# Kernel optimization log

Hardware: AMD Instinct MI355X
Metric: run time of the kernel (lower is better)

Reference implementation:

```python
import jax, jax.numpy as jnp
import numpy as np

DN = ('NCHW', 'OIHW', 'NCHW')
B, HP, LR = 4, 256, 64  # batch, pan side length, lrms side length


def conv(x, w):
    return jax.lax.conv_general_dilated(x, w, (1, 1), 'SAME', dimension_numbers=DN)


def gauss_k(ks, sigma):
    i = np.arange(ks) - (ks - 1) / 2.0
    k = np.exp(-(i * i) / (2.0 * sigma * sigma))
    k /= k.sum()
    return jnp.asarray(k, jnp.float32)


def gaussian_hp(x, ks, sigma):
    # Faithful to source: cv2.GaussianBlur is applied ONLY to channel 0 of each
    # sample; remaining channels get lp == x, hence hp == 0. Separable blur with
    # reflect-101 padding (cv2 default border).
    k = gauss_k(ks, sigma)
    p = ks // 2
    x0 = x[:, :1]
    y = jnp.pad(x0, ((0, 0), (0, 0), (p, p), (0, 0)), mode='reflect')
    y = jax.lax.conv_general_dilated(y, k.reshape(1, 1, ks, 1), (1, 1), 'VALID', dimension_numbers=DN)
    y = jnp.pad(y, ((0, 0), (0, 0), (0, 0), (p, p)), mode='reflect')
    y = jax.lax.conv_general_dilated(y, k.reshape(1, 1, 1, ks), (1, 1), 'VALID', dimension_numbers=DN)
    hp0 = x0 - y
    if x.shape[1] > 1:
        hp0 = jnp.concatenate([hp0, jnp.zeros_like(x[:, 1:])], axis=1)
    return hp0


def pixel_shuffle(x, r):
    b, c, h, w = x.shape
    x = x.reshape(b, c // (r * r), r, r, h, w)
    return x.transpose(0, 1, 4, 2, 5, 3).reshape(b, c // (r * r), h * r, w * r)


def hornet(x, w1, w2):
    return conv(jax.nn.gelu(conv(x, w1)), w2)


def ffc(x, wl2l, wl2g, wg2l, wspec):
    # ratio 0.5/0.5 split -> 8 local / 8 global channels
    xl, xg = x[:, :8], x[:, 8:]
    l2l, l2g, g2l = conv(xl, wl2l), conv(xl, wl2g), conv(xg, wg2l)
    f = jnp.fft.rfft2(xg, axes=(2, 3), norm='ortho')
    z = jnp.concatenate([f.real, f.imag], axis=1)
    z = jax.nn.relu(conv(z, wspec))
    g2g = jnp.fft.irfft2(z[:, :8] + 1j * z[:, 8:], s=xg.shape[2:], axes=(2, 3), norm='ortho')
    return l2l, l2g, g2l, g2g


def refine(x, win, wb1, wb2, wca1, wca2, wout):
    # RCAB-style refinement: conv-in, residual body with channel attention, conv-out
    y = conv(x, win)
    bdy = conv(jax.nn.relu(conv(y, wb1)), wb2)
    ca = jax.nn.sigmoid(conv(jax.nn.relu(conv(bdy.mean((2, 3), keepdims=True), wca1)), wca2))
    return conv(y + bdy * ca, wout)


def coord1d(n):
    r = 1.0 / n
    return -1.0 + r + 2.0 * r * jnp.arange(n, dtype=jnp.float32)


def mlp(x, w_in, b_in, w_h, b_h, w_out, b_out):
    h = jax.nn.relu(x @ w_in + b_in)
    for i in range(w_h.shape[0]):
        h = jax.nn.relu(h @ w_h[i] + b_h[i])
    return h @ w_out + b_out


def liif(feat, coord, cell, w_in, b_in, w_h, b_h, w_out, b_out):
    # LIIF with feat_unfold=True, local_ensemble=True, cell_decode=True
    b, c, h, w = feat.shape
    fp = jnp.pad(feat, ((0, 0), (0, 0), (1, 1), (1, 1)))
    patches = jnp.concatenate([fp[:, :, i:i + h, j:j + w] for i in range(3) for j in range(3)], axis=1)
    pf = patches.reshape(b, 9 * c, h * w)  # [B, 144, H*W]
    cy, cx = coord1d(h), coord1d(w)
    rx, ry = 1.0 / h, 1.0 / w
    preds, areas = [], []
    for vx in (-1.0, 1.0):
        for vy in (-1.0, 1.0):
            c0 = jnp.clip(coord[..., 0] + vx * rx + 1e-6, -1 + 1e-6, 1 - 1e-6)
            c1 = jnp.clip(coord[..., 1] + vy * ry + 1e-6, -1 + 1e-6, 1 - 1e-6)
            i0 = jnp.clip(jnp.floor((c0 + 1.0) * h / 2.0).astype(jnp.int32), 0, h - 1)
            i1 = jnp.clip(jnp.floor((c1 + 1.0) * w / 2.0).astype(jnp.int32), 0, w - 1)
            idx = i0 * w + i1  # [B, Q]
            q = jnp.take_along_axis(pf, idx[:, None, :], axis=2).transpose(0, 2, 1)  # [B,Q,144]
            rel0 = (coord[..., 0] - cy[i0]) * h
            rel1 = (coord[..., 1] - cx[i1]) * w
            inp = jnp.concatenate([q, rel0[..., None], rel1[..., None],
                                   cell[..., :1] * h, cell[..., 1:] * w], axis=-1)
            preds.append(mlp(inp, w_in, b_in, w_h, b_h, w_out, b_out))
            areas.append(jnp.abs(rel0 * rel1) + 1e-9)
    areas[0], areas[3] = areas[3], areas[0]
    areas[1], areas[2] = areas[2], areas[1]
    tot = areas[0] + areas[1] + areas[2] + areas[3]
    return sum(p * (a / tot)[..., None] for p, a in zip(preds, areas))


def _forward(lrms, pan, w_conv_ps, hor_w1, hor_w2, ffc_l2l, ffc_l2g, ffc_g2l, ffc_spec,
             ref_in, ref_b1, ref_b2, ref_ca1, ref_ca2, ref_out,
             w_fuse, w_liif, w_hp, mlp_w_in, mlp_b_in, mlp_w_h, mlp_b_h, mlp_w_out, mlp_b_out):
    side = pan.shape[-1]
    c1 = coord1d(side)
    grid = jnp.stack(jnp.meshgrid(c1, c1, indexing='ij'), -1).reshape(-1, 2)
    coord = jnp.broadcast_to(grid[None], (pan.shape[0], side * side, 2))
    cell = jnp.full_like(coord, 2.0 / side)

    lrms_up = pixel_shuffle(conv(lrms, w_conv_ps), 4)

    blur_cfg = [(5, 1.5), (27, 2.0), (41, 2.8)]
    R = lambda i: (ref_in[i], ref_b1[i], ref_b2[i], ref_ca1[i], ref_ca2[i], ref_out[i])
    Fc = lambda i: (ffc_l2l[i], ffc_l2g[i], ffc_g2l[i], ffc_spec[i])

    fused = []
    for br in range(3):
        ks, sg = blur_cfg[br]
        feat = jnp.concatenate([gaussian_hp(pan, ks, sg), gaussian_hp(lrms_up, ks, sg)], axis=1)
        feat = hornet(feat, hor_w1[br], hor_w2[br])
        f0 = refine(feat, *R(3 * br))
        l2l, l2g, g2l, g2g = ffc(f0, *Fc(2 * br))
        f1 = refine(jnp.concatenate([l2g + g2g, l2l + g2l], axis=1), *R(3 * br + 1))
        l2l, l2g, g2l, g2g = ffc(f1, *Fc(2 * br + 1))
        f2 = refine(jnp.concatenate([l2g + g2g, l2l + g2l], axis=1), *R(3 * br + 2))
        fused.append(conv(jnp.concatenate([f0, f1, f2], axis=1), w_fuse[br]))

    feat_all = conv(jnp.concatenate(fused, axis=1), w_liif)
    fo = liif(feat_all, coord, cell, mlp_w_in, mlp_b_in, mlp_w_h, mlp_b_h, mlp_w_out, mlp_b_out)
    fo = fo.transpose(0, 2, 1).reshape(pan.shape[0], -1, side, side)
    return conv(fo, w_hp) + lrms_up


def setup_inputs() -> dict:
    key = jax.random.key(0)
    ks = jax.random.split(key, 24)
    n = lambda i, shape, s=0.05: jax.random.normal(ks[i], shape, jnp.float32) * s
    return dict(
        lrms=n(0, (B, 4, LR, LR), 1.0),
        pan=n(1, (B, 1, HP, HP), 1.0),
        w_conv_ps=n(2, (64, 4, 3, 3)),
        hor_w1=n(3, (3, 16, 5, 3, 3)),
        hor_w2=n(4, (3, 16, 16, 3, 3)),
        ffc_l2l=n(5, (6, 8, 8, 3, 3)),
        ffc_l2g=n(6, (6, 8, 8, 3, 3)),
        ffc_g2l=n(7, (6, 8, 8, 3, 3)),
        ffc_spec=n(8, (6, 16, 16, 1, 1), 0.1),
        ref_in=n(9, (9, 16, 16, 3, 3)),
        ref_b1=n(10, (9, 16, 16, 3, 3)),
        ref_b2=n(11, (9, 16, 16, 3, 3)),
        ref_ca1=n(12, (9, 4, 16, 1, 1), 0.1),
        ref_ca2=n(13, (9, 16, 4, 1, 1), 0.1),
        ref_out=n(14, (9, 16, 16, 3, 3)),
        w_fuse=n(15, (3, 16, 48, 1, 1), 0.1),
        w_liif=n(16, (16, 48, 1, 1), 0.1),
        w_hp=n(17, (4, 16, 3, 3)),
        mlp_w_in=n(18, (148, 256), 148 ** -0.5),
        mlp_b_in=jnp.zeros((256,), jnp.float32),
        mlp_w_h=n(19, (3, 256, 256), 256 ** -0.5),
        mlp_b_h=jnp.zeros((3, 256), jnp.float32),
        mlp_w_out=n(20, (256, 16), 256 ** -0.5),
        mlp_b_out=jnp.zeros((16,), jnp.float32),
    )


def reference(lrms, pan, w_conv_ps, hor_w1, hor_w2, ffc_l2l, ffc_l2g, ffc_g2l, ffc_spec,
              ref_in, ref_b1, ref_b2, ref_ca1, ref_ca2, ref_out,
              w_fuse, w_liif, w_hp, mlp_w_in, mlp_b_in, mlp_w_h, mlp_b_h, mlp_w_out, mlp_b_out):
    return _forward(lrms, pan, w_conv_ps, hor_w1, hor_w2, ffc_l2l, ffc_l2g, ffc_g2l, ffc_spec,
                    ref_in, ref_b1, ref_b2, ref_ca1, ref_ca2, ref_out,
                    w_fuse, w_liif, w_hp, mlp_w_in, mlp_b_in, mlp_w_h, mlp_b_h, mlp_w_out, mlp_b_out)
```

## Files before the change

### kernel.cpp

```cpp
#include <hip/hip_runtime.h>
#include <hip/hip_bf16.h>
#include <math.h>

typedef __hip_bfloat16 bf16;
typedef __attribute__((ext_vector_type(8))) short short8;
typedef __attribute__((ext_vector_type(4))) short short4v;
typedef __attribute__((ext_vector_type(4))) float float4v;

#define ACT_NONE 0
#define ACT_RELU 1
#define ACT_GELU 2

__device__ __forceinline__ float b2f(bf16 v){ return __bfloat162float(v); }
__device__ __forceinline__ bf16  f2b(float f){ return __float2bfloat16(f); }
__device__ __forceinline__ short f2bs(float f){ bf16 h = __float2bfloat16(f); return *reinterpret_cast<short*>(&h); }
__device__ __forceinline__ float bs2f(short s){ return __uint_as_float(((unsigned)(unsigned short)s) << 16); }
__device__ __forceinline__ void rotc(float& tr, float& ti, float cr, float ci){
    float t = tr*cr - ti*ci; ti = tr*ci + ti*cr; tr = t;
}

struct GK3 { float k[3][41]; int ks[3]; };

__global__ __launch_bounds__(256) void conv_ps_k(const float* __restrict__ lrms,
                                                 const float* __restrict__ w,
                                                 float* __restrict__ up){
    int tid = threadIdx.x, bx = blockIdx.x;
    int y = bx & 255, c = (bx >> 8) & 3, b = bx >> 10;
    int x = tid;
    int h = y >> 2, r1 = y & 3, ww = x >> 2, r2 = x & 3;
    int oc = c*16 + r1*4 + r2;
    float acc = 0.f;
    for (int ic = 0; ic < 4; ++ic) {
        const float* base = lrms + ((b*4 + ic) << 12);
        const float* wb = w + (oc*4 + ic)*9;
        #pragma unroll
        for (int ky = 0; ky < 3; ++ky) {
            int hh = h + ky - 1; if (hh < 0 || hh > 63) continue;
            #pragma unroll
            for (int kx = 0; kx < 3; ++kx) {
                int cc = ww + kx - 1; if (cc < 0 || cc > 63) continue;
                acc += base[(hh<<6) + cc] * wb[ky*3 + kx];
            }
        }
    }
    up[(((size_t)(b*4 + c)) << 16) + (y<<8) + x] = acc;
}

__global__ __launch_bounds__(256) void gauss_hp_k(const float* __restrict__ pan,
                                                  const float* __restrict__ lrms_up,
                                                  bf16* __restrict__ feat2, GK3 g){
    int tid = threadIdx.x, bx = blockIdx.x;
    int y = bx & 255, b = (bx >> 8) & 3, src = (bx >> 10) & 1, br = bx >> 11;
    int ks = g.ks[br], p = ks >> 1;
    const float* gk = g.k[br];
    const float* s = src ? (lrms_up + (size_t)b*4*65536) : (pan + (size_t)b*65536);
    __shared__ float vext[296];
    for (int i = tid; i < 296; i += 256) {
        int xe = i - 20; int xr = xe < 0 ? -xe : (xe > 255 ? 510 - xe : xe);
        float acc = 0.f;
        for (int t = 0; t < ks; ++t) {
            int yy = y - p + t; yy = yy < 0 ? -yy : (yy > 255 ? 510 - yy : yy);
            acc += gk[t] * s[(yy<<8) + xr];
        }
        vext[i] = acc;
    }
    __syncthreads();
    int x = tid;
    float acc = 0.f;
    for (int t = 0; t < ks; ++t) acc += gk[t] * vext[x - p + t + 20];
    float o = s[(y<<8) + x];
    feat2[(((size_t)((br*4 + b)*2 + src)) << 16) + (y<<8) + x] = f2b(o - acc);
}

__global__ __launch_bounds__(256) void convA_k(const bf16* __restrict__ in, int inCper, int Cin,
                                               const float* __restrict__ wbase, int wbrstride, int wocstride,
                                               bf16* __restrict__ out, int act){
    int tid = threadIdx.x, bx = blockIdx.x;
    int y = bx & 255, b = (bx >> 8) & 3, br = bx >> 10;
    const float* w = wbase + (size_t)br * wbrstride;
    int x = tid;
    float acc[16];
    #pragma unroll
    for (int oc = 0; oc < 16; ++oc) acc[oc] = 0.f;
    for (int ic = 0; ic < Cin; ++ic) {
        const bf16* base = in + ((size_t)((br*4 + b)*inCper + ic) << 16);
        const float* wic = w + ic*9;
        #pragma unroll
        for (int ky = 0; ky < 3; ++ky) {
            int yy = y + ky - 1; if (yy < 0 || yy > 255) continue;
            const bf16* rowp = base + (yy<<8);
            float v0 = (x > 0)   ? b2f(rowp[x-1]) : 0.f;
            float v1 = b2f(rowp[x]);
            float v2 = (x < 255) ? b2f(rowp[x+1]) : 0.f;
            const float* wr = wic + ky*3;
            #pragma unroll
            for (int oc = 0; oc < 16; ++oc) {
                const float* wo = wr + oc*wocstride;
                acc[oc] = fmaf(wo[0], v0, fmaf(wo[1], v1, fmaf(wo[2], v2, acc[oc])));
            }
        }
    }
    #pragma unroll
    for (int oc = 0; oc < 16; ++oc) {
        float a = acc[oc];
        if (act == ACT_RELU) a = fmaxf(a, 0.f);
        else if (act == ACT_GELU) {
            float u = 0.7978845608028654f * (a + 0.044715f*a*a*a);
            a = 0.5f * a * (1.f + tanhf(u));
        }
        out[((size_t)((br*4 + b)*16 + oc) << 16) + (y<<8) + x] = f2b(a);
    }
}

__global__ __launch_bounds__(256) void pack_all_k(const float* __restrict__ mw_in,
        const float* __restrict__ mw_h, const float* __restrict__ mw_out,
        const float* __restrict__ hor_w2,
        const float* __restrict__ ref_in, const float* __restrict__ ref_b1,
        const float* __restrict__ ref_b2, const float* __restrict__ ref_out,
        const float* __restrict__ l2l, const float* __restrict__ l2g,
        const float* __restrict__ g2l,
        short* __restrict__ wp, short* __restrict__ wc){
    int idx = blockIdx.x*256 + threadIdx.x;
    const int S0 = 40960, SH = 65536;
    const int TOTM = S0 + 3*SH + 4096;
    const int TOTC = 45*2560;
    if (idx < TOTM) {
        float val;
        if (idx < S0) {
            int j = idx & 7, l = (idx>>3) & 63, nt = (idx>>9) & 15, kt = idx >> 13;
            int k = kt*32 + (l>>4)*8 + j;
            int n = nt*16 + (l&15);
            val = (k < 148) ? mw_in[k*256 + n] : 0.f;
        } else if (idx < S0 + 3*SH) {
            int i2 = idx - S0;
            int L = i2 >> 16, r = i2 & 65535;
            int j = r & 7, l = (r>>3) & 63, nt = (r>>9) & 15, kt = r >> 13;
            int k = kt*32 + (l>>4)*8 + j;
            int n = nt*16 + (l&15);
            val = mw_h[L*65536 + k*256 + n];
        } else {
            int i3 = idx - S0 - 3*SH;
            int j = i3 & 7, l = (i3>>3) & 63, kt = i3 >> 9;
            int k = kt*32 + (l>>4)*8 + j;
            int oc = l & 15;
            val = mw_out[k*16 + oc];
// ... 13 lines not shown
        int tap = k >> 4, ic = k & 15;
        if (g == 10 || g == 11) {
            int wi = 2*br + (g-10);
            if (n < 8) v = (ic < 8) ? l2g[((wi*8 + n)*8 + ic)*9 + tap] : 0.f;
            else {
                int o = n - 8;
                v = (ic < 8) ? l2l[((wi*8 + o)*8 + ic)*9 + tap]
                             : g2l[((wi*8 + o)*8 + (ic-8))*9 + tap];
            }
        } else {
            int widx = (n*16 + ic)*9 + tap;
            const float* src;
            if (g == 0)       src = hor_w2 + br*2304;
            else if (g <= 3)  src = ref_in + (3*br + (g-1))*2304;
            else if (g <= 6)  src = ref_b1 + (3*br + (g-4))*2304;
            else if (g <= 9)  src = ref_b2 + (3*br + (g-7))*2304;
            else              src = ref_out + (3*br + (g-12))*2304;
            v = src[widx];
        }
    }
    wc[idx2] = f2bs(v);
}

__global__ __launch_bounds__(256) void convM_k(const bf16* __restrict__ in,
        const short* __restrict__ wgroup,
        bf16* __restrict__ out, int act, float* __restrict__ means){
    __shared__ short sIn[6*258*20];
    __shared__ float sm[4][16];
    int tid = threadIdx.x, bx = blockIdx.x;
    int y0 = (bx & 63) << 2, b = (bx >> 6) & 3, br = bx >> 8;
    size_t pbase = (size_t)((br*4 + b)*16) << 16;
    if (tid < 192) {
        int r = tid >> 5, side = (tid >> 4) & 1, ic = tid & 15;
        sIn[(r*258 + (side ? 257 : 0))*20 + ic] = 0;
    }
    {
        int g = tid >> 5, tl = tid & 31, x0 = tl << 3, ic0 = g*2;
        for (int r = 0; r < 6; ++r) {
            int yy = y0 - 1 + r;
            short8 lo = {0,0,0,0,0,0,0,0}, hi = {0,0,0,0,0,0,0,0};
            if (yy >= 0 && yy <= 255) {
                lo = *(const short8*)&in[pbase + ((size_t)ic0<<16) + (yy<<8) + x0];
                hi = *(const short8*)&in[pbase + ((size_t)(ic0+1)<<16) + (yy<<8) + x0];
            }
            #pragma unroll
            for (int t = 0; t < 8; ++t) {
// ... 169 lines not shown
    }
    #pragma unroll
    for (int mt = 0; mt < 16; ++mt) {
        short8 a2 = {0,0,0,0,0,0,0,0};
        if (q < 2) a2 = *(const short8*)&sF[(mt*16 + m_l)*16 + q*8];
        float4v d2 = (float4v){0.f,0.f,0.f,0.f};
        d2 = __builtin_amdgcn_mfma_f32_16x16x32_bf16(a2, b2, d2, 0, 0, 0);
        size_t fidx = ((size_t)(b*48 + br*16 + m_l) << 16) + (yrow<<8) + mt*16 + q*4;
        short4v pk;
        if (step == 0) {
            #pragma unroll
            for (int r = 0; r < 4; ++r) pk[r] = f2bs(d2[r]);
        } else {
            short4v old = *(const short4v*)&fusedCat[fidx];
            #pragma unroll
            for (int r = 0; r < 4; ++r) pk[r] = f2bs(bs2f(old[r]) + d2[r]);
        }
        *(short4v*)&fusedCat[fidx] = pk;
    }
}

__global__ __launch_bounds__(256) void rfft_wT_k(const bf16* __restrict__ F,
                                                 bf16* __restrict__ ore, bf16* __restrict__ oim){
    __shared__ float rows[16][256];
    __shared__ float Ar[256], Ai[256];
    __shared__ float Tr[129][17], Ti[129][17];
    int tid = threadIdx.x, bx = blockIdx.x;
    int t = bx & 15, c = (bx >> 4) & 7, b = (bx >> 7) & 3, br = bx >> 9;
    int y0 = t << 4;
    size_t plane = (size_t)((br*4 + b)*16 + 8 + c) << 16;
    #pragma unroll
    for (int r = 0; r < 16; ++r)
        rows[r][tid] = b2f(F[plane + ((size_t)(y0 + r) << 8) + tid]);
    __syncthreads();
    int n1 = tid >> 4, k1 = tid & 15;
    float a1 = -6.283185307179586f * (float)k1 / 16.f;
    float c1, s1; __sincosf(a1, &s1, &c1);
    float a2 = -6.283185307179586f * (float)tid / 256.f;
    float c2v, s2v; __sincosf(a2, &s2v, &c2v);
    for (int r = 0; r < 16; ++r) {
        float twr = 1.f, twi = 0.f, ar = 0.f, ai = 0.f;
        #pragma unroll
        for (int n2 = 0; n2 < 16; ++n2) {
            float xr = rows[r][n1 + (n2<<4)];
            ar = fmaf(xr, twr, ar); ai = fmaf(xr, twi, ai);
            rotc(twr, twi, c1, s1);
        }
        Ar[tid] = ar; Ai[tid] = ai;
        __syncthreads();
        float t2r = 1.f, t2i = 0.f, re = 0.f, im = 0.f;
        #pragma unroll
        for (int m = 0; m < 16; ++m) {
            float rr = Ar[(m<<4) + k1], ii = Ai[(m<<4) + k1];
            re += rr*t2r - ii*t2i; im += ii*t2r + rr*t2i;
            rotc(t2r, t2i, c2v, s2v);
        }
        if (tid < 129) { Tr[tid][r] = re * 0.0625f; Ti[tid][r] = im * 0.0625f; }
        __syncthreads();
    }
    size_t obase = ((size_t)(((br*4 + b)*8 + c)*129)) * 256 + y0;
    for (int idx = tid; idx < 129*16; idx += 256) {
        int k = idx >> 4, ty = idx & 15;
        ore[obase + (size_t)k*256 + ty] = f2b(Tr[k][ty]);
        oim[obase + (size_t)k*256 + ty] = f2b(Ti[k][ty]);
    }
}

__global__ __launch_bounds__(256) void fftspec_hT_k(const bf16* __restrict__ re0, const bf16* __restrict__ im0,
                                                    const float* __restrict__ wspec, int step,
                                                    bf16* __restrict__ re1, bf16* __restrict__ im1){
    __shared__ float Fr[8][256], Fi[8][256], Sr[8][256], Si[8][256], Ar[256], Ai[256];
    int tid = threadIdx.x, bx = blockIdx.x;
    int k = bx % 129; int r2 = bx / 129; int b = r2 & 3, br = r2 >> 2;
    size_t cb = (size_t)((br*4 + b)*8) * 33024 + (size_t)k * 256;
    int n1 = tid >> 4, k1 = tid & 15;
    float a1 = -6.283185307179586f * (float)k1 / 16.f;
    float c1, s1; __sincosf(a1, &s1, &c1);
    float a2 = -6.283185307179586f * (float)tid / 256.f;
    float c2v, s2v; __sincosf(a2, &s2v, &c2v);
    #pragma unroll
    for (int c = 0; c < 8; ++c) {
        size_t base = cb + (size_t)c*33024 + tid;
        Fr[c][tid] = b2f(re0[base]);
        Fi[c][tid] = b2f(im0[base]);
    }
    __syncthreads();
    for (int c = 0; c < 8; ++c) {
        float twr = 1.f, twi = 0.f, ar = 0.f, ai = 0.f;
        #pragma unroll
        for (int n2 = 0; n2 < 16; ++n2) {
            float r = Fr[c][n1 + (n2<<4)], i = Fi[c][n1 + (n2<<4)];
            ar += r*twr - i*twi; ai += i*twr + r*twi;
            rotc(twr, twi, c1, s1);
        }
        Ar[tid] = ar; Ai[tid] = ai;
        __syncthreads();
        float t2r = 1.f, t2i = 0.f, rr = 0.f, ii = 0.f;
        #pragma unroll
        for (int m = 0; m < 16; ++m) {
            float r = Ar[(m<<4) + k1], i = Ai[(m<<4) + k1];
            rr += r*t2r - i*t2i; ii += i*t2r + r*t2i;
            rotc(t2r, t2i, c2v, s2v);
        }
        Sr[c][tid] = rr * 0.0625f; Si[c][tid] = ii * 0.0625f;
        __syncthreads();
    }
    {
        const float* wl = wspec + (2*br + step)*256;
        float outv[16];
        #pragma unroll
        for (int oc = 0; oc < 16; ++oc) {
            float acc = 0.f;
            #pragma unroll
            for (int ic = 0; ic < 8; ++ic)
                acc += Sr[ic][tid] * wl[oc*16 + ic] + Si[ic][tid] * wl[oc*16 + 8 + ic];
            outv[oc] = fmaxf(acc, 0.f);
        }
        __syncthreads();
        #pragma unroll
        for (int oc = 0; oc < 8; ++oc) { Fr[oc][tid] = outv[oc]; Fi[oc][tid] = outv[oc+8]; }
        __syncthreads();
    }
    for (int c = 0; c < 8; ++c) {
        float twr = 1.f, twi = 0.f, ar = 0.f, ai = 0.f;
        #pragma unroll
        for (int n2 = 0; n2 < 16; ++n2) {
            float r = Fr[c][n1 + (n2<<4)], i = Fi[c][n1 + (n2<<4)];
            ar += r*twr + i*twi;
            ai += i*twr - r*twi;
            rotc(twr, twi, c1, s1);
        }
        Ar[tid] = ar; Ai[tid] = ai;
        __syncthreads();
        float t2r = 1.f, t2i = 0.f, rr = 0.f, ii = 0.f;
        #pragma unroll
        for (int m = 0; m < 16; ++m) {
            float r = Ar[(m<<4) + k1], i = Ai[(m<<4) + k1];
            rr += r*t2r + i*t2i;
            ii += i*t2r - r*t2i;
            rotc(t2r, t2i, c2v, s2v);
        }
        size_t base = cb + (size_t)c*33024 + tid;
        re1[base] = f2b(rr * 0.0625f);
        im1[base] = f2b(ii * 0.0625f);
        __syncthreads();
    }
}

__global__ __launch_bounds__(256) void irfft_wT_k(const bf16* __restrict__ re1, const bf16* __restrict__ im1,
                                                  bf16* __restrict__ A){
    __shared__ float Cr[129][17], Ci[129][17];
    __shared__ float er[256], ei[256];
    __shared__ float Ar[256], Ai[256];
    int tid = threadIdx.x, bx = blockIdx.x;
    int t = bx & 15, c = (bx >> 4) & 7, b = (bx >> 7) & 3, br = bx >> 9;
    int y0 = t << 4;
    size_t ibase = ((size_t)(((br*4 + b)*8 + c)*129)) * 256 + y0;
    for (int idx = tid; idx < 129*16; idx += 256) {
        int k = idx >> 4, ty = idx & 15;
        Cr[k][ty] = b2f(re1[ibase + (size_t)k*256 + ty]);
        Ci[k][ty] = (k == 0 || k == 128) ? 0.f : b2f(im1[ibase + (size_t)k*256 + ty]);
    }
    __syncthreads();
    int n1 = tid >> 4, k1 = tid & 15;
    float a1 = 6.283185307179586f * (float)k1 / 16.f;
    float c1, s1; __sincosf(a1, &s1, &c1);
    float a2 = 6.283185307179586f * (float)tid / 256.f;
    float c2v, s2v; __sincosf(a2, &s2v, &c2v);
    size_t plane = (size_t)((br*4 + b)*16 + c) << 16;
    for (int ty = 0; ty < 16; ++ty) {
        if (tid < 129) { er[tid] = Cr[tid][ty]; ei[tid] = Ci[tid][ty]; }
        else           { er[tid] = Cr[256 - tid][ty]; ei[tid] = -Ci[256 - tid][ty]; }
        __syncthreads();
        float twr = 1.f, twi = 0.f, ar = 0.f, ai = 0.f;
        #pragma unroll
        for (int n2 = 0; n2 < 16; ++n2) {
            float r = er[n1 + (n2<<4)], i = ei[n1 + (n2<<4)];
            ar += r*twr - i*twi; ai += i*twr + r*twi;
            rotc(twr, twi, c1, s1);
        }
        Ar[tid] = ar; Ai[tid] = ai;
        __syncthreads();
        float t2r = 1.f, t2i = 0.f, racc = 0.f;
        #pragma unroll
        for (int m = 0; m < 16; ++m) {
            float r = Ar[(m<<4) + k1], i = Ai[(m<<4) + k1];
            racc += r*t2r - i*t2i;
            rotc(t2r, t2i, c2v, s2v);
        }
        size_t o = plane + ((size_t)(y0 + ty) << 8) + tid;
        A[o] = f2b(b2f(A[o]) + racc * 0.0625f);
        __syncthreads();
    }
}

__global__ __launch_bounds__(256) void fuse1x1_k(const bf16* __restrict__ fc, const float* __restrict__ wl,
                                                 bf16* __restrict__ feat_all){
    int tid = threadIdx.x, bx = blockIdx.x;
    int pt = bx & 255, b = bx >> 8;
    int p = (pt << 8) + tid;
    float acc[16];
    #pragma unroll
    for (int oc = 0; oc < 16; ++oc) acc[oc] = 0.f;
    for (int ic = 0; ic < 48; ++ic) {
        float v = b2f(fc[((size_t)(b*48 + ic) << 16) + p]);
        #pragma unroll
        for (int oc = 0; oc < 16; ++oc) acc[oc] = fmaf(wl[oc*48 + ic], v, acc[oc]);
    }
    #pragma unroll
    for (int oc = 0; oc < 16; ++oc)
        feat_all[((size_t)(b*16 + oc) << 16) + p] = f2b(acc[oc]);
}

__global__ __launch_bounds__(256) void mlp_mfma_k(const short* __restrict__ feat,
        const short* __restrict__ wp,
        const float* __restrict__ b_in, const float* __restrict__ b_h,
        const float* __restrict__ b_out,
        float* __restrict__ fo){
    extern __shared__ short act_s[];
    int tid = threadIdx.x, bx = blockIdx.x;
    long P0 = (long)bx * 64;
    for (int idx = tid; idx < 64*160; idx += 256) {
        int pp = idx / 160, j = idx - pp*160;
        long P = P0 + pp;
        int bb = (int)(P >> 16), pim = (int)(P & 65535);
        int s0 = pim >> 8, s1 = pim & 255;
        short v = 0;
        if (j < 144) {
            int iy = j/48, ix = (j>>4)%3, c2 = j&15;
            int yy = s0 + iy - 1, xx = s1 + ix - 1;
            if (yy >= 0 && yy < 256 && xx >= 0 && xx < 256)
                v = feat[(((long)(bb*16 + c2)) << 16) + (yy<<8) + xx];
        } else if (j == 146 || j == 147) v = 0x4000;
        act_s[pp*264 + j] = v;
    }
    __syncthreads();

    int l = tid & 63, w = tid >> 6;
    int m_l = l & 15, q = l >> 4;
    int ntb = w*4;
    const short* wph  = wp + 40960;
    const short* wpo  = wp + 40960 + 3*65536;

    float4v acc[4][4];
    #pragma unroll
    for (int mt = 0; mt < 4; ++mt)
        #pragma unroll
        for (int nt = 0; nt < 4; ++nt) acc[mt][nt] = (float4v){0.f,0.f,0.f,0.f};
    for (int kt = 0; kt < 5; ++kt) {
        const short* bp = wp + ((size_t)(kt*16 + ntb)*64 + l)*8;
        short8 bfr[4];
        #pragma unroll
        for (int nt = 0; nt < 4; ++nt) bfr[nt] = *(const short8*)(bp + (size_t)nt*64*8);
        #pragma unroll
        for (int mt = 0; mt < 4; ++mt) {
            short8 a = *(const short8*)&act_s[(mt*16 + m_l)*264 + kt*32 + q*8];
            #pragma unroll
            for (int nt = 0; nt < 4; ++nt)
                acc[mt][nt] = __builtin_amdgcn_mfma_f32_16x16x32_bf16(a, bfr[nt], acc[mt][nt], 0, 0, 0);
        }
    }
    __syncthreads();
    #pragma unroll
    for (int nt = 0; nt < 4; ++nt) {
        int n = (ntb + nt)*16 + m_l;
        float bias = b_in[n];
        #pragma unroll
        for (int mt = 0; mt < 4; ++mt)
            #pragma unroll
            for (int r = 0; r < 4; ++r) {
                float vv = fmaxf(acc[mt][nt][r] + bias, 0.f);
                act_s[(mt*16 + q*4 + r)*264 + n] = f2bs(vv);
            }
    }
    __syncthreads();
    for (int L = 0; L < 3; ++L) {
        #pragma unroll
        for (int mt = 0; mt < 4; ++mt)
            #pragma unroll
            for (int nt = 0; nt < 4; ++nt) acc[mt][nt] = (float4v){0.f,0.f,0.f,0.f};
        const short* wl = wph + (size_t)L * 65536;
        for (int kt = 0; kt < 8; ++kt) {
            const short* bp = wl + ((size_t)(kt*16 + ntb)*64 + l)*8;
            short8 bfr[4];
            #pragma unroll
            for (int nt = 0; nt < 4; ++nt) bfr[nt] = *(const short8*)(bp + (size_t)nt*64*8);
            #pragma unroll
            for (int mt = 0; mt < 4; ++mt) {
                short8 a = *(const short8*)&act_s[(mt*16 + m_l)*264 + kt*32 + q*8];
                #pragma unroll
                for (int nt = 0; nt < 4; ++nt)
                    acc[mt][nt] = __builtin_amdgcn_mfma_f32_16x16x32_bf16(a, bfr[nt], acc[mt][nt], 0, 0, 0);
            }
        }
        __syncthreads();
        #pragma unroll
        for (int nt = 0; nt < 4; ++nt) {
            int n = (ntb + nt)*16 + m_l;
            float bias = b_h[L*256 + n];
            #pragma unroll
            for (int mt = 0; mt < 4; ++mt)
                #pragma unroll
                for (int r = 0; r < 4; ++r) {
                    float vv = fmaxf(acc[mt][nt][r] + bias, 0.f);
                    act_s[(mt*16 + q*4 + r)*264 + n] = f2bs(vv);
                }
        }
        __syncthreads();
    }
    if (w == 0) {
        float4v o[4];
        #pragma unroll
        for (int mt = 0; mt < 4; ++mt) o[mt] = (float4v){0.f,0.f,0.f,0.f};
        for (int kt = 0; kt < 8; ++kt) {
            short8 bf = *(const short8*)(wpo + ((size_t)kt*64 + l)*8);
// ... 22 lines not shown
        const short* __restrict__ wp,
        const float* __restrict__ b_in, const float* __restrict__ b_h,
        const float* __restrict__ b_out,
        float* __restrict__ fo){
    extern __shared__ short act_s[];
    int tid = threadIdx.x, bx = blockIdx.x;
    int E0 = bx * 128;
    for (int idx = tid; idx < 128*160; idx += 256) {
        int pp = idx / 160, j = idx - pp*160;
        int e = E0 + pp; if (e >= 6132) e = 0;
        int bb = e / 1533; int rem = e - bb*1533;
        int cn = rem / 511; int eidx = rem - cn*511;
        int s0 = (eidx < 256) ? 255 : eidx - 256;
        int s1 = (eidx < 256) ? eidx : 255;
        int vx = (cn == 0) ? -1 : 1;
        int vy = (cn == 1) ? -1 : 1;
        int i0 = (vx > 0) ? min(s0+1, 255) : s0;
        int i1 = (vy > 0) ? min(s1+1, 255) : s1;
        short v = 0;
        if (j < 144) {
            int iy = j/48, ix = (j>>4)%3, c2 = j&15;
            int yy = i0 + iy - 1, xx = i1 + ix - 1;
            if (yy >= 0 && yy < 256 && xx >= 0 && xx < 256)
                v = feat[(((long)(bb*16 + c2)) << 16) + (yy<<8) + xx];
        } else if (j == 144) v = f2bs(2.f*(float)(s0 - i0));
        else if (j == 145) v = f2bs(2.f*(float)(s1 - i1));
        else if (j >= 146) v = 0x4000;
        act_s[pp*264 + j] = v;
    }
    __syncthreads();

    int l = tid & 63, w = tid >> 6;
    int m_l = l & 15, q = l >> 4;
    int row0 = w * 32;
    const short* wph  = wp + 40960;
    const short* wpo  = wp + 40960 + 3*65536;

    float4v acc[2][16];
    #pragma unroll
    for (int mt = 0; mt < 2; ++mt)
        #pragma unroll
        for (int nt = 0; nt < 16; ++nt) acc[mt][nt] = (float4v){0.f,0.f,0.f,0.f};
    for (int kt = 0; kt < 5; ++kt) {
        short8 a0 = *(const short8*)&act_s[(row0 + m_l)*264 + kt*32 + q*8];
        short8 a1 = *(const short8*)&act_s[(row0 + 16 + m_l)*264 + kt*32 + q*8];
        const short* bp = wp + ((size_t)(kt*16)*64 + l)*8;
        #pragma unroll
// ... 125 lines not shown

    const size_t PLANE = 65536;
    char* base = (char*)d_ws;
    size_t off = 0;
    auto alloc = [&](size_t bytes){ void* p = base + off; off += (bytes + 255) & ~(size_t)255; return p; };
    float* lrms_up  = (float*)alloc(16*PLANE*4);
    bf16*  feat2    = (bf16*) alloc(24*PLANE*2);
    bf16*  bA       = (bf16*) alloc(192*PLANE*2);
    bf16*  bB       = (bf16*) alloc(192*PLANE*2);
    bf16*  bC       = (bf16*) alloc(192*PLANE*2);
    bf16*  bF       = (bf16*) alloc(192*PLANE*2);
    bf16*  fusedCat = (bf16*) alloc(192*PLANE*2);
    bf16*  feat_all = (bf16*) alloc(64*PLANE*2);
    float* fo       = (float*)alloc(64*PLANE*4);
    const size_t FFTB = (size_t)3*4*8*256*129;
    bf16* re0 = (bf16*)alloc(FFTB*2); bf16* im0 = (bf16*)alloc(FFTB*2);
    bf16* re1 = (bf16*)alloc(FFTB*2); bf16* im1 = (bf16*)alloc(FFTB*2);
    short* wpack = (short*)alloc(241664*2);
    short* wconv = (short*)alloc(45*2560*2);
    float* means3 = (float*)alloc(3*192*4);
    if (off > ws_size) return;

    hipMemsetAsync(means3, 0, 3*192*4, stream);
    pack_all_k<<<dim3(1395), dim3(256), 0, stream>>>(mw_in, mw_h, mw_out, hor_w2,
        ref_in, ref_b1, ref_b2, ref_out, ffc_l2l, ffc_l2g, ffc_g2l, wpack, wconv);
    conv_ps_k<<<dim3(4096), dim3(256), 0, stream>>>(lrms, w_convps, lrms_up);

    GK3 g3;
    {
        const int kss[3] = {5, 27, 41};
        const double sgs[3] = {1.5, 2.0, 2.8};
        for (int br = 0; br < 3; ++br) {
            g3.ks[br] = kss[br];
            double tmp[41]; double s = 0.0; double c = (kss[br]-1)/2.0;
            for (int i = 0; i < kss[br]; ++i) { double d = i - c; tmp[i] = exp(-(d*d)/(2.0*sgs[br]*sgs[br])); s += tmp[i]; }
            for (int i = 0; i < 41; ++i) g3.k[br][i] = (i < kss[br]) ? (float)(tmp[i]/s) : 0.f;
        }
    }
    gauss_hp_k<<<dim3(6144), dim3(256), 0, stream>>>(pan, lrms_up, feat2, g3);

    convA_k<<<dim3(3072), dim3(256), 0, stream>>>(feat2, 2, 2, hor_w1, 720, 45, bA, ACT_GELU);
    convM_k<<<dim3(768), dim3(256), 0, stream>>>(bA, wconv + 0*3*2560, bB, ACT_NONE, nullptr);

    for (int step = 0; step < 3; ++step) {
        bf16* Xin = (step == 0) ? bB : bA;
        bf16* Yb  = (step == 0) ? bA : bB;
        bf16* Db  = (step == 0) ? bB : bA;
        convM_k<<<dim3(768), dim3(256), 0, stream>>>(Xin, wconv + (1+step)*3*2560, Yb, ACT_NONE, nullptr);
        convM_k<<<dim3(768), dim3(256), 0, stream>>>(Yb,  wconv + (4+step)*3*2560, bC, ACT_RELU, nullptr);
        convM_k<<<dim3(768), dim3(256), 0, stream>>>(bC,  wconv + (7+step)*3*2560, Db, ACT_NONE, means3 + step*192);
        convOutM_k<<<dim3(768), dim3(256), 0, stream>>>(Yb, Db, means3 + step*192, ref_ca1, ref_ca2,
                                                        wconv + (12+step)*3*2560, w_fuse, step, bF, fusedCat);
        if (step < 2) {
            convM_k<<<dim3(768), dim3(256), 0, stream>>>(bF, wconv + (10+step)*3*2560, bA, ACT_NONE, nullptr);
            rfft_wT_k<<<dim3(1536), dim3(256), 0, stream>>>(bF, re0, im0);
            fftspec_hT_k<<<dim3(1548), dim3(256), 0, stream>>>(re0, im0, ffc_spec, step, re1, im1);
            irfft_wT_k<<<dim3(1536), dim3(256), 0, stream>>>(re1, im1, bA);
        }
    }

    fuse1x1_k<<<dim3(1024), dim3(256), 0, stream>>>(fusedCat, w_liif, feat_all);
    mlp_mfma_k<<<dim3(4096), dim3(256), 64*264*2, stream>>>((const short*)feat_all, wpack, mb_in, mb_h, mb_out, fo);
    mlp_edge_mfma_k<<<dim3(48), dim3(256), 128*264*2, stream>>>((const short*)feat_all, wpack, mb_in, mb_h, mb_out, fo);
    final_k<<<dim3(4096), dim3(256), 0, stream>>>(fo, w_hp, lrms_up, out);
}
```

Measured before the change: 1.169 ms.

## Merge init kernels, batch FFT stages, store features channel-last, prefetch MLP weights

```diff
diff --git a/kernel.cpp b/kernel.cpp
--- a/kernel.cpp
+++ b/kernel.cpp
@@ -21,106 +21,39 @@
 
 struct GK3 { float k[3][41]; int ks[3]; };
 
-__global__ __launch_bounds__(256) void conv_ps_k(const float* __restrict__ lrms,
-                                                 const float* __restrict__ w,
-                                                 float* __restrict__ up){
-    int tid = threadIdx.x, bx = blockIdx.x;
-    int y = bx & 255, c = (bx >> 8) & 3, b = bx >> 10;
-    int x = tid;
-    int h = y >> 2, r1 = y & 3, ww = x >> 2, r2 = x & 3;
-    int oc = c*16 + r1*4 + r2;
-    float acc = 0.f;
-    for (int ic = 0; ic < 4; ++ic) {
-        const float* base = lrms + ((b*4 + ic) << 12);
-        const float* wb = w + (oc*4 + ic)*9;
-        #pragma unroll
-        for (int ky = 0; ky < 3; ++ky) {
-            int hh = h + ky - 1; if (hh < 0 || hh > 63) continue;
-            #pragma unroll
-            for (int kx = 0; kx < 3; ++kx) {
-                int cc = ww + kx - 1; if (cc < 0 || cc > 63) continue;
-                acc += base[(hh<<6) + cc] * wb[ky*3 + kx];
-            }
-        }
-    }
-    up[(((size_t)(b*4 + c)) << 16) + (y<<8) + x] = acc;
-}
-
-__global__ __launch_bounds__(256) void gauss_hp_k(const float* __restrict__ pan,
-                                                  const float* __restrict__ lrms_up,
-                                                  bf16* __restrict__ feat2, GK3 g){
-    int tid = threadIdx.x, bx = blockIdx.x;
-    int y = bx & 255, b = (bx >> 8) & 3, src = (bx >> 10) & 1, br = bx >> 11;
-    int ks = g.ks[br], p = ks >> 1;
-    const float* gk = g.k[br];
-    const float* s = src ? (lrms_up + (size_t)b*4*65536) : (pan + (size_t)b*65536);
-    __shared__ float vext[296];
-    for (int i = tid; i < 296; i += 256) {
-        int xe = i - 20; int xr = xe < 0 ? -xe : (xe > 255 ? 510 - xe : xe);
-        float acc = 0.f;
-        for (int t = 0; t < ks; ++t) {
-            int yy = y - p + t; yy = yy < 0 ? -yy : (yy > 255 ? 510 - yy : yy);
-            acc += gk[t] * s[(yy<<8) + xr];
-        }
-        vext[i] = acc;
-    }
-    __syncthreads();
-    int x = tid;
-    float acc = 0.f;
-    for (int t = 0; t < ks; ++t) acc += gk[t] * vext[x - p + t + 20];
-    float o = s[(y<<8) + x];
-    feat2[(((size_t)((br*4 + b)*2 + src)) << 16) + (y<<8) + x] = f2b(o - acc);
-}
-
-__global__ __launch_bounds__(256) void convA_k(const bf16* __restrict__ in, int inCper, int Cin,
-                                               const float* __restrict__ wbase, int wbrstride, int wocstride,
-                                               bf16* __restrict__ out, int act){
-    int tid = threadIdx.x, bx = blockIdx.x;
-    int y = bx & 255, b = (bx >> 8) & 3, br = bx >> 10;
-    const float* w = wbase + (size_t)br * wbrstride;
-    int x = tid;
-    float acc[16];
-    #pragma unroll
-    for (int oc = 0; oc < 16; ++oc) acc[oc] = 0.f;
-    for (int ic = 0; ic < Cin; ++ic) {
-        const bf16* base = in + ((size_t)((br*4 + b)*inCper + ic) << 16);
-        const float* wic = w + ic*9;
-        #pragma unroll
-        for (int ky = 0; ky < 3; ++ky) {
-            int yy = y + ky - 1; if (yy < 0 || yy > 255) continue;
-            const bf16* rowp = base + (yy<<8);
-            float v0 = (x > 0)   ? b2f(rowp[x-1]) : 0.f;
-            float v1 = b2f(rowp[x]);
-            float v2 = (x < 255) ? b2f(rowp[x+1]) : 0.f;
-            const float* wr = wic + ky*3;
-            #pragma unroll
-            for (int oc = 0; oc < 16; ++oc) {
-                const float* wo = wr + oc*wocstride;
-                acc[oc] = fmaf(wo[0], v0, fmaf(wo[1], v1, fmaf(wo[2], v2, acc[oc])));
-            }
-        }
-    }
-    #pragma unroll
-    for (int oc = 0; oc < 16; ++oc) {
-        float a = acc[oc];
-        if (act == ACT_RELU) a = fmaxf(a, 0.f);
-        else if (act == ACT_GELU) {
-            float u = 0.7978845608028654f * (a + 0.044715f*a*a*a);
-            a = 0.5f * a * (1.f + tanhf(u));
-        }
-        out[((size_t)((br*4 + b)*16 + oc) << 16) + (y<<8) + x] = f2b(a);
-    }
-}
-
-__global__ __launch_bounds__(256) void pack_all_k(const float* __restrict__ mw_in,
-        const float* __restrict__ mw_h, const float* __restrict__ mw_out,
-        const float* __restrict__ hor_w2,
+__global__ __launch_bounds__(256) void init_k(const float* __restrict__ lrms,
+        const float* __restrict__ wps, float* __restrict__ up,
+        const float* __restrict__ mw_in, const float* __restrict__ mw_h,
+        const float* __restrict__ mw_out, const float* __restrict__ hor_w2,
         const float* __restrict__ ref_in, const float* __restrict__ ref_b1,
         const float* __restrict__ ref_b2, const float* __restrict__ ref_out,
         const float* __restrict__ l2l, const float* __restrict__ l2g,
         const float* __restrict__ g2l,
         short* __restrict__ wp, short* __restrict__ wc){
-    int idx = blockIdx.x*256 + threadIdx.x;
+    int tid = threadIdx.x, bx = blockIdx.x;
+    if (bx < 4096) {
+        int y = bx & 255, c = (bx >> 8) & 3, b = bx >> 10;
+        int x = tid;
+        int h = y >> 2, r1 = y & 3, ww = x >> 2, r2 = x & 3;
+        int oc = c*16 + r1*4 + r2;
+        float acc = 0.f;
+        for (int ic = 0; ic < 4; ++ic) {
+            const float* base = lrms + ((b*4 + ic) << 12);
+            const float* wb = wps + (oc*4 + ic)*9;
+            #pragma unroll
+            for (int ky = 0; ky < 3; ++ky) {
+                int hh = h + ky - 1; if (hh < 0 || hh > 63) continue;
+                #pragma unroll
+                for (int kx = 0; kx < 3; ++kx) {
+                    int cc = ww + kx - 1; if (cc < 0 || cc > 63) continue;
+                    acc += base[(hh<<6) + cc] * wb[ky*3 + kx];
+                }
+            }
+        }
+        up[(((size_t)(b*4 + c)) << 16) + (y<<8) + x] = acc;
+        return;
+    }
+    int idx = (bx - 4096)*256 + tid;
     const int S0 = 40960, SH = 65536;
     const int TOTM = S0 + 3*SH + 4096;
     const int TOTC = 45*2560;
@@ -180,6 +113,72 @@
     wc[idx2] = f2bs(v);
 }
 
+__global__ __launch_bounds__(256) void gauss_hp_k(const float* __restrict__ pan,
+                                                  const float* __restrict__ lrms_up,
+                                                  bf16* __restrict__ feat2, GK3 g){
+    int tid = threadIdx.x, bx = blockIdx.x;
+    int y = bx & 255, b = (bx >> 8) & 3, src = (bx >> 10) & 1, br = bx >> 11;
+    int ks = g.ks[br], p = ks >> 1;
+    const float* gk = g.k[br];
+    const float* s = src ? (lrms_up + (size_t)b*4*65536) : (pan + (size_t)b*65536);
+    __shared__ float vext[296];
+    for (int i = tid; i < 296; i += 256) {
+        int xe = i - 20; int xr = xe < 0 ? -xe : (xe > 255 ? 510 - xe : xe);
+        float acc = 0.f;
+        for (int t = 0; t < ks; ++t) {
+            int yy = y - p + t; yy = yy < 0 ? -yy : (yy > 255 ? 510 - yy : yy);
+            acc += gk[t] * s[(yy<<8) + xr];
+        }
+        vext[i] = acc;
+    }
+    __syncthreads();
+    int x = tid;
+    float acc = 0.f;
+    for (int t = 0; t < ks; ++t) acc += gk[t] * vext[x - p + t + 20];
+    float o = s[(y<<8) + x];
+    feat2[(((size_t)((br*4 + b)*2 + src)) << 16) + (y<<8) + x] = f2b(o - acc);
+}
+
+__global__ __launch_bounds__(256) void convA_k(const bf16* __restrict__ in, int inCper, int Cin,
+                                               const float* __restrict__ wbase, int wbrstride, int wocstride,
+                                               bf16* __restrict__ out, int act){
+    int tid = threadIdx.x, bx = blockIdx.x;
+    int y = bx & 255, b = (bx >> 8) & 3, br = bx >> 10;
+    const float* w = wbase + (size_t)br * wbrstride;
+    int x = tid;
+    float acc[16];
+    #pragma unroll
+    for (int oc = 0; oc < 16; ++oc) acc[oc] = 0.f;
+    for (int ic = 0; ic < Cin; ++ic) {
+        const bf16* base = in + ((size_t)((br*4 + b)*inCper + ic) << 16);
+        const float* wic = w + ic*9;
+        #pragma unroll
+        for (int ky = 0; ky < 3; ++ky) {
+            int yy = y + ky - 1; if (yy < 0 || yy > 255) continue;
+            const bf16* rowp = base + (yy<<8);
+            float v0 = (x > 0)   ? b2f(rowp[x-1]) : 0.f;
+            float v1 = b2f(rowp[x]);
+            float v2 = (x < 255) ? b2f(rowp[x+1]) : 0.f;
+            const float* wr = wic + ky*3;
+            #pragma unroll
+            for (int oc = 0; oc < 16; ++oc) {
+                const float* wo = wr + oc*wocstride;
+                acc[oc] = fmaf(wo[0], v0, fmaf(wo[1], v1, fmaf(wo[2], v2, acc[oc])));
+            }
+        }
+    }
+    #pragma unroll
+    for (int oc = 0; oc < 16; ++oc) {
+        float a = acc[oc];
+        if (act == ACT_RELU) a = fmaxf(a, 0.f);
+        else if (act == ACT_GELU) {
+            float u = 0.7978845608028654f * (a + 0.044715f*a*a*a);
+            a = 0.5f * a * (1.f + tanhf(u));
+        }
+        out[((size_t)((br*4 + b)*16 + oc) << 16) + (y<<8) + x] = f2b(a);
+    }
+}
+
 __global__ __launch_bounds__(256) void convM_k(const bf16* __restrict__ in,
         const short* __restrict__ wgroup,
         bf16* __restrict__ out, int act, float* __restrict__ means){
@@ -395,9 +394,11 @@
 
 __global__ __launch_bounds__(256) void rfft_wT_k(const bf16* __restrict__ F,
                                                  bf16* __restrict__ ore, bf16* __restrict__ oim){
-    __shared__ float rows[16][256];
-    __shared__ float Ar[256], Ai[256];
-    __shared__ float Tr[129][17], Ti[129][17];
+    __shared__ float ubuf[4386];
+    extern __shared__ float2 Acx[];
+    float (*rows)[256] = (float(*)[256])ubuf;
+    float (*Tr)[17] = (float(*)[17])ubuf;
+    float (*Ti)[17] = (float(*)[17])(ubuf + 129*17);
     int tid = threadIdx.x, bx = blockIdx.x;
     int t = bx & 15, c = (bx >> 4) & 7, b = (bx >> 7) & 3, br = bx >> 9;
     int y0 = t << 4;
@@ -409,8 +410,6 @@
     int n1 = tid >> 4, k1 = tid & 15;
     float a1 = -6.283185307179586f * (float)k1 / 16.f;
     float c1, s1; __sincosf(a1, &s1, &c1);
-    float a2 = -6.283185307179586f * (float)tid / 256.f;
-    float c2v, s2v; __sincosf(a2, &s2v, &c2v);
     for (int r = 0; r < 16; ++r) {
         float twr = 1.f, twi = 0.f, ar = 0.f, ai = 0.f;
         #pragma unroll
@@ -419,18 +418,25 @@
             ar = fmaf(xr, twr, ar); ai = fmaf(xr, twi, ai);
             rotc(twr, twi, c1, s1);
         }
-        Ar[tid] = ar; Ai[tid] = ai;
-        __syncthreads();
-        float t2r = 1.f, t2i = 0.f, re = 0.f, im = 0.f;
-        #pragma unroll
-        for (int m = 0; m < 16; ++m) {
-            float rr = Ar[(m<<4) + k1], ii = Ai[(m<<4) + k1];
-            re += rr*t2r - ii*t2i; im += ii*t2r + rr*t2i;
-            rotc(t2r, t2i, c2v, s2v);
-        }
-        if (tid < 129) { Tr[tid][r] = re * 0.0625f; Ti[tid][r] = im * 0.0625f; }
-        __syncthreads();
-    }
+        Acx[r*256 + tid] = make_float2(ar, ai);
+    }
+    __syncthreads();
+    if (tid < 129) {
+        int kk1 = tid & 15;
+        float a2 = -6.283185307179586f * (float)tid / 256.f;
+        float c2v, s2v; __sincosf(a2, &s2v, &c2v);
+        for (int r = 0; r < 16; ++r) {
+            float t2r = 1.f, t2i = 0.f, re = 0.f, im = 0.f;
+            #pragma unroll
+            for (int m = 0; m < 16; ++m) {
+                float2 A = Acx[r*256 + (m<<4) + kk1];
+                re += A.x*t2r - A.y*t2i; im += A.y*t2r + A.x*t2i;
+                rotc(t2r, t2i, c2v, s2v);
+            }
+            Tr[tid][r] = re * 0.0625f; Ti[tid][r] = im * 0.0625f;
+        }
+    }
+    __syncthreads();
     size_t obase = ((size_t)(((br*4 + b)*8 + c)*129)) * 256 + y0;
     for (int idx = tid; idx < 129*16; idx += 256) {
         int k = idx >> 4, ty = idx & 15;
@@ -442,7 +448,8 @@
 __global__ __launch_bounds__(256) void fftspec_hT_k(const bf16* __restrict__ re0, const bf16* __restrict__ im0,
                                                     const float* __restrict__ wspec, int step,
                                                     bf16* __restrict__ re1, bf16* __restrict__ im1){
-    __shared__ float Fr[8][256], Fi[8][256], Sr[8][256], Si[8][256], Ar[256], Ai[256];
+    __shared__ float2 Fc[8][256];
+    __shared__ float2 Sc[8][256];
     int tid = threadIdx.x, bx = blockIdx.x;
     int k = bx % 129; int r2 = bx / 129; int b = r2 & 3, br = r2 >> 2;
     size_t cb = (size_t)((br*4 + b)*8) * 33024 + (size_t)k * 256;
@@ -454,30 +461,31 @@
     #pragma unroll
     for (int c = 0; c < 8; ++c) {
         size_t base = cb + (size_t)c*33024 + tid;
-        Fr[c][tid] = b2f(re0[base]);
-        Fi[c][tid] = b2f(im0[base]);
+        Fc[c][tid] = make_float2(b2f(re0[base]), b2f(im0[base]));
     }
     __syncthreads();
     for (int c = 0; c < 8; ++c) {
         float twr = 1.f, twi = 0.f, ar = 0.f, ai = 0.f;
         #pragma unroll
         for (int n2 = 0; n2 < 16; ++n2) {
-            float r = Fr[c][n1 + (n2<<4)], i = Fi[c][n1 + (n2<<4)];
-            ar += r*twr - i*twi; ai += i*twr + r*twi;
+            float2 x = Fc[c][n1 + (n2<<4)];
+            ar += x.x*twr - x.y*twi; ai += x.y*twr + x.x*twi;
             rotc(twr, twi, c1, s1);
         }
-        Ar[tid] = ar; Ai[tid] = ai;
-        __syncthreads();
+        Sc[c][tid] = make_float2(ar, ai);
+    }
+    __syncthreads();
+    for (int c = 0; c < 8; ++c) {
         float t2r = 1.f, t2i = 0.f, rr = 0.f, ii = 0.f;
         #pragma unroll
         for (int m = 0; m < 16; ++m) {
-            float r = Ar[(m<<4) + k1], i = Ai[(m<<4) + k1];
-            rr += r*t2r - i*t2i; ii += i*t2r + r*t2i;
+            float2 A = Sc[c][(m<<4) + k1];
+            rr += A.x*t2r - A.y*t2i; ii += A.y*t2r + A.x*t2i;
             rotc(t2r, t2i, c2v, s2v);
         }
-        Sr[c][tid] = rr * 0.0625f; Si[c][tid] = ii * 0.0625f;
-        __syncthreads();
-    }
+        Fc[c][tid] = make_float2(rr * 0.0625f, ii * 0.0625f);
+    }
+    __syncthreads();
     {
         const float* wl = wspec + (2*br + step)*256;
         float outv[16];
@@ -485,85 +493,88 @@
         for (int oc = 0; oc < 16; ++oc) {
             float acc = 0.f;
             #pragma unroll
-            for (int ic = 0; ic < 8; ++ic)
-                acc += Sr[ic][tid] * wl[oc*16 + ic] + Si[ic][tid] * wl[oc*16 + 8 + ic];
+            for (int ic = 0; ic < 8; ++ic) {
+                float2 gv = Fc[ic][tid];
+                acc += gv.x * wl[oc*16 + ic] + gv.y * wl[oc*16 + 8 + ic];
+            }
             outv[oc] = fmaxf(acc, 0.f);
         }
         __syncthreads();
         #pragma unroll
-        for (int oc = 0; oc < 8; ++oc) { Fr[oc][tid] = outv[oc]; Fi[oc][tid] = outv[oc+8]; }
-        __syncthreads();
-    }
+        for (int oc = 0; oc < 8; ++oc) Sc[oc][tid] = make_float2(outv[oc], outv[oc+8]);
+    }
+    __syncthreads();
     for (int c = 0; c < 8; ++c) {
         float twr = 1.f, twi = 0.f, ar = 0.f, ai = 0.f;
         #pragma unroll
         for (int n2 = 0; n2 < 16; ++n2) {
-            float r = Fr[c][n1 + (n2<<4)], i = Fi[c][n1 + (n2<<4)];
-            ar += r*twr + i*twi;
-            ai += i*twr - r*twi;
+            float2 x = Sc[c][n1 + (n2<<4)];
+            ar += x.x*twr + x.y*twi;
+            ai += x.y*twr - x.x*twi;
             rotc(twr, twi, c1, s1);
         }
-        Ar[tid] = ar; Ai[tid] = ai;
-        __syncthreads();
+        Fc[c][tid] = make_float2(ar, ai);
+    }
+    __syncthreads();
+    for (int c = 0; c < 8; ++c) {
         float t2r = 1.f, t2i = 0.f, rr = 0.f, ii = 0.f;
         #pragma unroll
         for (int m = 0; m < 16; ++m) {
-            float r = Ar[(m<<4) + k1], i = Ai[(m<<4) + k1];
-            rr += r*t2r + i*t2i;
-            ii += i*t2r - r*t2i;
+            float2 A = Fc[c][(m<<4) + k1];
+            rr += A.x*t2r + A.y*t2i;
+            ii += A.y*t2r - A.x*t2i;
             rotc(t2r, t2i, c2v, s2v);
         }
         size_t base = cb + (size_t)c*33024 + tid;
         re1[base] = f2b(rr * 0.0625f);
         im1[base] = f2b(ii * 0.0625f);
-        __syncthreads();
     }
 }
 
 __global__ __launch_bounds__(256) void irfft_wT_k(const bf16* __restrict__ re1, const bf16* __restrict__ im1,
                                                   bf16* __restrict__ A){
-    __shared__ float Cr[129][17], Ci[129][17];
-    __shared__ float er[256], ei[256];
-    __shared__ float Ar[256], Ai[256];
+    __shared__ float2 Ecx[16][258];
+    extern __shared__ float2 Acx[];
     int tid = threadIdx.x, bx = blockIdx.x;
     int t = bx & 15, c = (bx >> 4) & 7, b = (bx >> 7) & 3, br = bx >> 9;
     int y0 = t << 4;
     size_t ibase = ((size_t)(((br*4 + b)*8 + c)*129)) * 256 + y0;
-    for (int idx = tid; idx < 129*16; idx += 256) {
-        int k = idx >> 4, ty = idx & 15;
-        Cr[k][ty] = b2f(re1[ibase + (size_t)k*256 + ty]);
-        Ci[k][ty] = (k == 0 || k == 128) ? 0.f : b2f(im1[ibase + (size_t)k*256 + ty]);
+    for (int idx = tid; idx < 16*256; idx += 256) {
+        int i = idx >> 4, ty = idx & 15;
+        int k = (i < 129) ? i : 256 - i;
+        float re = b2f(re1[ibase + (size_t)k*256 + ty]);
+        float im = (k == 0 || k == 128) ? 0.f : b2f(im1[ibase + (size_t)k*256 + ty]);
+        if (i >= 129) im = -im;
+        Ecx[ty][i] = make_float2(re, im);
     }
     __syncthreads();
     int n1 = tid >> 4, k1 = tid & 15;
     float a1 = 6.283185307179586f * (float)k1 / 16.f;
     float c1, s1; __sincosf(a1, &s1, &c1);
+    for (int ty = 0; ty < 16; ++ty) {
+        float twr = 1.f, twi = 0.f, ar = 0.f, ai = 0.f;
+        #pragma unroll
+        for (int n2 = 0; n2 < 16; ++n2) {
+            float2 x = Ecx[ty][n1 + (n2<<4)];
+            ar += x.x*twr - x.y*twi; ai += x.y*twr + x.x*twi;
+            rotc(twr, twi, c1, s1);
+        }
+        Acx[ty*256 + tid] = make_float2(ar, ai);
+    }
+    __syncthreads();
     float a2 = 6.283185307179586f * (float)tid / 256.f;
     float c2v, s2v; __sincosf(a2, &s2v, &c2v);
     size_t plane = (size_t)((br*4 + b)*16 + c) << 16;
     for (int ty = 0; ty < 16; ++ty) {
-        if (tid < 129) { er[tid] = Cr[tid][ty]; ei[tid] = Ci[tid][ty]; }
-        else           { er[tid] = Cr[256 - tid][ty]; ei[tid] = -Ci[256 - tid][ty]; }
-        __syncthreads();
-        float twr = 1.f, twi = 0.f, ar = 0.f, ai = 0.f;
-        #pragma unroll
-        for (int n2 = 0; n2 < 16; ++n2) {
-            float r = er[n1 + (n2<<4)], i = ei[n1 + (n2<<4)];
-            ar += r*twr - i*twi; ai += i*twr + r*twi;
-            rotc(twr, twi, c1, s1);
-        }
-        Ar[tid] = ar; Ai[tid] = ai;
-        __syncthreads();
         float t2r = 1.f, t2i = 0.f, racc = 0.f;
         #pragma unroll
         for (int m = 0; m < 16; ++m) {
-            float r = Ar[(m<<4) + k1], i = Ai[(m<<4) + k1];
-            racc += r*t2r - i*t2i;
+            float2 Av = Acx[ty*256 + (m<<4) + k1];
+            racc += Av.x*t2r - Av.y*t2i;
             rotc(t2r, t2i, c2v, s2v);
         }
         size_t o = plane + ((size_t)(y0 + ty) << 8) + tid;
         A[o] = f2b(b2f(A[o]) + racc * 0.0625f);
-        __syncthreads();
     }
 }
 
@@ -580,9 +591,14 @@
         #pragma unroll
         for (int oc = 0; oc < 16; ++oc) acc[oc] = fmaf(wl[oc*48 + ic], v, acc[oc]);
     }
-    #pragma unroll
-    for (int oc = 0; oc < 16; ++oc)
-        feat_all[((size_t)(b*16 + oc) << 16) + p] = f2b(acc[oc]);
+    size_t obase = (((size_t)b << 16) + p) << 4;
+    #pragma unroll
+    for (int h = 0; h < 2; ++h) {
+        short8 pk;
+        #pragma unroll
+        for (int e = 0; e < 8; ++e) pk[e] = f2bs(acc[h*8 + e]);
+        *(short8*)&feat_all[obase + h*8] = pk;
+    }
 }
 
 __global__ __launch_bounds__(256) void mlp_mfma_k(const short* __restrict__ feat,
@@ -603,7 +619,7 @@
             int iy = j/48, ix = (j>>4)%3, c2 = j&15;
             int yy = s0 + iy - 1, xx = s1 + ix - 1;
             if (yy >= 0 && yy < 256 && xx >= 0 && xx < 256)
-                v = feat[(((long)(bb*16 + c2)) << 16) + (yy<<8) + xx];
+                v = feat[((((long)bb << 16) + (yy<<8) + xx) << 4) + c2];
         } else if (j == 146 || j == 147) v = 0x4000;
         act_s[pp*264 + j] = v;
     }
@@ -616,21 +632,32 @@
     const short* wpo  = wp + 40960 + 3*65536;
 
     float4v acc[4][4];
+    short8 bcur[4], bnxt[4];
     #pragma unroll
     for (int mt = 0; mt < 4; ++mt)
         #pragma unroll
         for (int nt = 0; nt < 4; ++nt) acc[mt][nt] = (float4v){0.f,0.f,0.f,0.f};
+    {
+        const short* bp = wp + ((size_t)ntb*64 + l)*8;
+        #pragma unroll
+        for (int nt = 0; nt < 4; ++nt) bcur[nt] = *(const short8*)(bp + (size_t)nt*512);
+    }
     for (int kt = 0; kt < 5; ++kt) {
-        const short* bp = wp + ((size_t)(kt*16 + ntb)*64 + l)*8;
-        short8 bfr[4];
-        #pragma unroll
-        for (int nt = 0; nt < 4; ++nt) bfr[nt] = *(const short8*)(bp + (size_t)nt*64*8);
+        if (kt < 4) {
+            const short* bp = wp + ((size_t)((kt+1)*16 + ntb)*64 + l)*8;
+            #pragma unroll
+            for (int nt = 0; nt < 4; ++nt) bnxt[nt] = *(const short8*)(bp + (size_t)nt*512);
+        }
         #pragma unroll
         for (int mt = 0; mt < 4; ++mt) {
             short8 a = *(const short8*)&act_s[(mt*16 + m_l)*264 + kt*32 + q*8];
             #pragma unroll
             for (int nt = 0; nt < 4; ++nt)
-                acc[mt][nt] = __builtin_amdgcn_mfma_f32_16x16x32_bf16(a, bfr[nt], acc[mt][nt], 0, 0, 0);
+                acc[mt][nt] = __builtin_amdgcn_mfma_f32_16x16x32_bf16(a, bcur[nt], acc[mt][nt], 0, 0, 0);
+        }
+        if (kt < 4) {
+            #pragma unroll
+            for (int nt = 0; nt < 4; ++nt) bcur[nt] = bnxt[nt];
         }
     }
     __syncthreads();
@@ -653,17 +680,27 @@
             #pragma unroll
             for (int nt = 0; nt < 4; ++nt) acc[mt][nt] = (float4v){0.f,0.f,0.f,0.f};
         const short* wl = wph + (size_t)L * 65536;
+        {
+            const short* bp = wl + ((size_t)ntb*64 + l)*8;
+            #pragma unroll
+            for (int nt = 0; nt < 4; ++nt) bcur[nt] = *(const short8*)(bp + (size_t)nt*512);
+        }
         for (int kt = 0; kt < 8; ++kt) {
-            const short* bp = wl + ((size_t)(kt*16 + ntb)*64 + l)*8;
-            short8 bfr[4];
-            #pragma unroll
-            for (int nt = 0; nt < 4; ++nt) bfr[nt] = *(const short8*)(bp + (size_t)nt*64*8);
+            if (kt < 7) {
+                const short* bp = wl + ((size_t)((kt+1)*16 + ntb)*64 + l)*8;
+                #pragma unroll
+                for (int nt = 0; nt < 4; ++nt) bnxt[nt] = *(const short8*)(bp + (size_t)nt*512);
+            }
             #pragma unroll
             for (int mt = 0; mt < 4; ++mt) {
                 short8 a = *(const short8*)&act_s[(mt*16 + m_l)*264 + kt*32 + q*8];
                 #pragma unroll
                 for (int nt = 0; nt < 4; ++nt)
-                    acc[mt][nt] = __builtin_amdgcn_mfma_f32_16x16x32_bf16(a, bfr[nt], acc[mt][nt], 0, 0, 0);
+                    acc[mt][nt] = __builtin_amdgcn_mfma_f32_16x16x32_bf16(a, bcur[nt], acc[mt][nt], 0, 0, 0);
+            }
+            if (kt < 7) {
+                #pragma unroll
+                for (int nt = 0; nt < 4; ++nt) bcur[nt] = bnxt[nt];
             }
         }
         __syncthreads();
@@ -732,7 +769,7 @@
             int iy = j/48, ix = (j>>4)%3, c2 = j&15;
             int yy = i0 + iy - 1, xx = i1 + ix - 1;
             if (yy >= 0 && yy < 256 && xx >= 0 && xx < 256)
-                v = feat[(((long)(bb*16 + c2)) << 16) + (yy<<8) + xx];
+                v = feat[((((long)bb << 16) + (yy<<8) + xx) << 4) + c2];
         } else if (j == 144) v = f2bs(2.f*(float)(s0 - i0));
         else if (j == 145) v = f2bs(2.f*(float)(s1 - i1));
         else if (j >= 146) v = 0x4000;
@@ -904,9 +941,9 @@
     if (off > ws_size) return;
 
     hipMemsetAsync(means3, 0, 3*192*4, stream);
-    pack_all_k<<<dim3(1395), dim3(256), 0, stream>>>(mw_in, mw_h, mw_out, hor_w2,
-        ref_in, ref_b1, ref_b2, ref_out, ffc_l2l, ffc_l2g, ffc_g2l, wpack, wconv);
-    conv_ps_k<<<dim3(4096), dim3(256), 0, stream>>>(lrms, w_convps, lrms_up);
+    init_k<<<dim3(4096 + 1395), dim3(256), 0, stream>>>(lrms, w_convps, lrms_up,
+        mw_in, mw_h, mw_out, hor_w2, ref_in, ref_b1, ref_b2, ref_out,
+        ffc_l2l, ffc_l2g, ffc_g2l, wpack, wconv);
 
     GK3 g3;
     {
@@ -935,9 +972,9 @@
                                                         wconv + (12+step)*3*2560, w_fuse, step, bF, fusedCat);
         if (step < 2) {
             convM_k<<<dim3(768), dim3(256), 0, stream>>>(bF, wconv + (10+step)*3*2560, bA, ACT_NONE, nullptr);
-            rfft_wT_k<<<dim3(1536), dim3(256), 0, stream>>>(bF, re0, im0);
+            rfft_wT_k<<<dim3(1536), dim3(256), 32768, stream>>>(bF, re0, im0);
             fftspec_hT_k<<<dim3(1548), dim3(256), 0, stream>>>(re0, im0, ffc_spec, step, re1, im1);
-            irfft_wT_k<<<dim3(1536), dim3(256), 0, stream>>>(re1, im1, bA);
+            irfft_wT_k<<<dim3(1536), dim3(256), 32768, stream>>>(re1, im1, bA);
         }
     }
 
```

Measured after the change: 1.190 ms. No clear change (+1.8%).
